# Performance work log

Measured on AMD Instinct MI355X. Metric: run time of the kernel, lower is better.

Reference implementation:

```python
import jax, jax.numpy as jnp
import numpy as np

N_NODES = 30000
N_EDGES = 480000
IN_FEAT = 256
OUT_FEAT = 256
N_RELS = 8
N_HEADS = 4
HEAD_DIM = OUT_FEAT // N_HEADS
LEAKY_SLOPE = 0.2


def setup_inputs() -> dict:
    key = jax.random.key(0)
    ks = jax.random.split(key, 8)
    inputs = jax.random.normal(ks[0], (N_NODES, IN_FEAT), dtype=jnp.float32)
    conv_weights = jax.random.normal(ks[1], (N_RELS, N_HEADS, IN_FEAT, HEAD_DIM), dtype=jnp.float32) * (1.0 / np.sqrt(IN_FEAT))
    attn_l = jax.random.normal(ks[2], (N_RELS, N_HEADS, HEAD_DIM), dtype=jnp.float32) * 0.1
    attn_r = jax.random.normal(ks[3], (N_RELS, N_HEADS, HEAD_DIM), dtype=jnp.float32) * 0.1
    h_bias = jax.random.normal(ks[4], (OUT_FEAT,), dtype=jnp.float32) * 0.02
    edge_src = jax.random.randint(ks[5], (N_EDGES,), 0, N_NODES, dtype=jnp.int32)
    edge_dst = jax.random.randint(ks[6], (N_EDGES,), 0, N_NODES, dtype=jnp.int32)
    edge_type = jax.random.randint(ks[7], (N_EDGES,), 0, N_RELS, dtype=jnp.int32)
    return {"inputs": inputs, "conv_weights": conv_weights, "attn_l": attn_l,
            "attn_r": attn_r, "h_bias": h_bias, "edge_src": edge_src,
            "edge_dst": edge_dst, "edge_type": edge_type}


def reference(inputs, conv_weights, attn_l, attn_r, h_bias, edge_src, edge_dst, edge_type):
    # Per-relation dense transform of all node features: [R, N, H, D]
    feat_all = jnp.einsum('ni,rhid->rnhd', inputs, conv_weights)
    # Gather transformed source/destination features per edge: [E, H, D]
    feat_src_e = feat_all[edge_type, edge_src]
    feat_dst_e = feat_all[edge_type, edge_dst]
    # Per-edge attention logits (relation-specific attn vectors): [E, H]
    el = jnp.sum(feat_src_e * attn_l[edge_type], axis=-1)
    er = jnp.sum(feat_dst_e * attn_r[edge_type], axis=-1)
    e = jax.nn.leaky_relu(el + er, negative_slope=LEAKY_SLOPE)
    # Segment softmax over incoming edges of each destination node
    m = jax.ops.segment_max(e, edge_dst, num_segments=N_NODES)  # [N, H]
    ex = jnp.exp(e - m[edge_dst])
    denom = jax.ops.segment_sum(ex, edge_dst, num_segments=N_NODES)  # [N, H]
    alpha = ex / denom[edge_dst]  # [E, H]
    # Attention-weighted aggregation of transformed source features
    h = jax.ops.segment_sum(alpha[..., None] * feat_src_e, edge_dst, num_segments=N_NODES)  # [N, H, D]
    h = h.reshape(N_NODES, OUT_FEAT) + h_bias
    # activation=None, self_loop=False, dropout=0.0 (eval) -> identity
    return h
```

## Files before the change

### kernel.cpp

```cpp
#include <hip/hip_runtime.h>

#define N_NODES 30000
#define NPAD    30080
#define N_EDGES 480000
#define N_RELS  8
#define NB_SCAN 118

typedef short bf16x8 __attribute__((ext_vector_type(8)));
typedef float f32x4  __attribute__((ext_vector_type(4)));

__device__ __forceinline__ unsigned short f2bf(float f) {
    unsigned u = __float_as_uint(f);
    u += 0x7fffu + ((u >> 16) & 1u);
    return (unsigned short)(u >> 16);
}
__device__ __forceinline__ float bf2f(unsigned short h) {
    return __uint_as_float(((unsigned)h) << 16);
}

__device__ __forceinline__ void load_lds16(const void* g, void* l) {
    __builtin_amdgcn_global_load_lds(
        (const __attribute__((address_space(1))) unsigned int*)g,
        (__attribute__((address_space(3))) unsigned int*)l,
        16, 0, 0);
}

__global__ void cast_x_kernel(const float* __restrict__ x, unsigned short* __restrict__ xbf) {
    int t = blockIdx.x * 256 + threadIdx.x;
    int base = t * 8;
    int n = base >> 8;
    unsigned short h[8];
    if (n < N_NODES) {
        float4 a = *(const float4*)(x + base);
        float4 b = *(const float4*)(x + base + 4);
        h[0]=f2bf(a.x); h[1]=f2bf(a.y); h[2]=f2bf(a.z); h[3]=f2bf(a.w);
        h[4]=f2bf(b.x); h[5]=f2bf(b.y); h[6]=f2bf(b.z); h[7]=f2bf(b.w);
    } else {
        #pragma unroll
        for (int i = 0; i < 8; ++i) h[i] = 0;
    }
    uint4 o;
    o.x = (unsigned)h[0] | ((unsigned)h[1] << 16);
    o.y = (unsigned)h[2] | ((unsigned)h[3] << 16);
    o.z = (unsigned)h[4] | ((unsigned)h[5] << 16);
    o.w = (unsigned)h[6] | ((unsigned)h[7] << 16);
    *(uint4*)(xbf + base) = o;
}

__global__ void wtrans_kernel(const float* __restrict__ cw, unsigned short* __restrict__ wt) {
    int o = blockIdx.x * 256 + threadIdx.x;
    if (o >= N_RELS * 256 * 256) return;
    int i = o & 255;
    int c = (o >> 8) & 255;
    int r = o >> 16;
    float v = cw[(((size_t)r * 4 + (c >> 6)) * 256 + i) * 64 + (c & 63)];
    wt[o] = f2bf(v);
}

__global__ void hist_kernel(const int* __restrict__ edst, int* __restrict__ counts) {
    int e = blockIdx.x * 256 + threadIdx.x;
    if (e < N_EDGES) atomicAdd(&counts[edst[e]], 1);
}

__global__ void scan1_kernel(const int* __restrict__ counts, int* __restrict__ locexcl,
                             int* __restrict__ bsum) {
    __shared__ int sm[256];
    int tid = threadIdx.x;
    int idx = blockIdx.x * 256 + tid;
    int v = (idx < N_NODES) ? counts[idx] : 0;
    sm[tid] = v;
    __syncthreads();
    for (int o = 1; o < 256; o <<= 1) {
        int t = (tid >= o) ? sm[tid - o] : 0;
        __syncthreads();
        sm[tid] += t;
        __syncthreads();
    }
    int incl = sm[tid];
    if (idx < N_NODES) locexcl[idx] = incl - v;
    if (tid == 255) bsum[blockIdx.x] = incl;
}

__global__ void scan2_kernel(const int* __restrict__ bsum, int* __restrict__ bpre) {
    __shared__ int sm[128];
    int tid = threadIdx.x;
    int v = (tid < NB_SCAN) ? bsum[tid] : 0;
    sm[tid] = v;
    __syncthreads();
    for (int o = 1; o < 128; o <<= 1) {
        int t = (tid >= o) ? sm[tid - o] : 0;
        __syncthreads();
        sm[tid] += t;
        __syncthreads();
    }
    if (tid < NB_SCAN) bpre[tid] = sm[tid] - v;
}

__global__ void scan3_kernel(const int* __restrict__ locexcl, const int* __restrict__ bpre,
                             int* __restrict__ offsets, int* __restrict__ cursor) {
    int idx = blockIdx.x * 256 + threadIdx.x;
    if (idx < N_NODES) {
        int o = bpre[blockIdx.x] + locexcl[idx];
        offsets[idx] = o;
        cursor[idx]  = o;
    }
    if (idx == 0) offsets[N_NODES] = N_EDGES;
}

__global__ __launch_bounds__(256) void gemm_kernel(
    const unsigned short* __restrict__ xbf,
    const unsigned short* __restrict__ wt,
    const float* __restrict__ attn_l,
    const float* __restrict__ attn_r,
    unsigned short* __restrict__ feat,
    float* __restrict__ projl,
    float* __restrict__ projr)
{
    __shared__ __align__(16) unsigned char smem[32768];

    const int tid  = threadIdx.x;
    const int lane = tid & 63;
    const int w    = tid >> 6;
    const int wm   = w >> 1;
    const int wn   = w & 1;
    const int quad = lane >> 4;
    const int l15  = lane & 15;

    const int bid = blockIdx.x;
    const int mt  = bid >> 4;
    const int r   = (bid >> 1) & 7;
    const int nt  = bid & 1;
    const int mbase = mt * 128;
    const int nbase = nt * 128;

    const unsigned short* Asrc = xbf + (size_t)mbase * 256;
    const unsigned short* Bsrc = wt + ((size_t)r * 256 + nbase) * 256;

    f32x4 acc[4][4] = {};

    const int srow = w * 16 + (lane >> 2);
    const int c0   = lane & 3;

    for (int k0 = 0; k0 < 256; k0 += 32) {
        #pragma unroll
        for (int n = 0; n < 2; ++n) {
            int row = n * 64 + srow;
            int c   = c0 ^ ((row >> 1) & 3);
            load_lds16(Asrc + (size_t)row * 256 + k0 + c * 8, smem + (n * 256 + w * 64) * 16);
        }
        #pragma unroll
        for (int n = 0; n < 2; ++n) {
            int row = n * 64 + srow;
            int c   = c0 ^ ((row >> 1) & 3);
            load_lds16(Bsrc + (size_t)row * 256 + k0 + c * 8, smem + 8192 + (n * 256 + w * 64) * 16);
        }
        __syncthreads();

        bf16x8 af[4], bfr[4];
        #pragma unroll
        for (int i = 0; i < 4; ++i) {
            int row = wm * 64 + i * 16 + l15;
            int cc  = quad ^ ((row >> 1) & 3);
            af[i] = *(const bf16x8*)(smem + row * 64 + cc * 16);
        }
        #pragma unroll
        for (int j = 0; j < 4; ++j) {
            int row = wn * 64 + j * 16 + l15;
            int cc  = quad ^ ((row >> 1) & 3);
            bfr[j] = *(const bf16x8*)(smem + 8192 + row * 64 + cc * 16);
        }

        #pragma unroll
        for (int i = 0; i < 4; ++i)
            #pragma unroll
            for (int j = 0; j < 4; ++j)
                acc[i][j] = __builtin_amdgcn_mfma_f32_16x16x32_bf16(af[i], bfr[j], acc[i][j], 0, 0, 0);
        __syncthreads();
    }

    size_t obase = ((size_t)r * NPAD + mbase + wm * 64) * 256 + nbase + wn * 64;
    #pragma unroll
    for (int i = 0; i < 4; ++i)
        #pragma unroll
        for (int j = 0; j < 4; ++j)
            #pragma unroll
            for (int e = 0; e < 4; ++e)
                feat[obase + (size_t)(i * 16 + quad * 4 + e) * 256 + j * 16 + l15] = f2bf(acc[i][j][e]);

    const int head = nt * 2 + wn;
    float al[4], ar[4];
    #pragma unroll
    for (int j = 0; j < 4; ++j) {
        al[j] = attn_l[((size_t)r * 4 + head) * 64 + j * 16 + l15];
        ar[j] = attn_r[((size_t)r * 4 + head) * 64 + j * 16 + l15];
    }
    float* bufL = (float*)smem + w * 1024;
    float* bufR = (float*)(smem + 16384) + w * 1024;
    #pragma unroll
    for (int i = 0; i < 4; ++i)
        #pragma unroll
        for (int e = 0; e < 4; ++e) {
            float s1 = 0.f, s2 = 0.f;
            #pragma unroll
            for (int j = 0; j < 4; ++j) {
                s1 += acc[i][j][e] * al[j];
                s2 += acc[i][j][e] * ar[j];
            }
            int row = i * 16 + quad * 4 + e;
            bufL[row * 16 + l15] = s1;
            bufR[row * 16 + l15] = s2;
        }
    float sL = 0.f, sR = 0.f;
    #pragma unroll
    for (int c = 0; c < 4; ++c) {
        float4 vl = *(const float4*)(bufL + lane * 16 + c * 4);
        float4 vr = *(const float4*)(bufR + lane * 16 + c * 4);
        sL += (vl.x + vl.y) + (vl.z + vl.w);
        sR += (vr.x + vr.y) + (vr.z + vr.w);
    }
    int g = mbase + wm * 64 + lane;
    projl[((size_t)r * NPAD + g) * 4 + head] = sL;
    projr[((size_t)r * NPAD + g) * 4 + head] = sR;
}

__global__ void logits_scatter_kernel(
    const int* __restrict__ esrc, const int* __restrict__ edst, const int* __restrict__ etyp,
    const float* __restrict__ projl, const float* __restrict__ projr,
    int* __restrict__ cursor, int* __restrict__ srcoff, float* __restrict__ exw)
{
    int e = blockIdx.x * 256 + threadIdx.x;
    if (e >= N_EDGES) return;
    int s = esrc[e], d = edst[e], t = etyp[e];
    float4 pl = ((const float4*)projl)[(size_t)t * NPAD + s];
    float4 pr = ((const float4*)projr)[(size_t)t * NPAD + d];
    float4 o;
    float v;
    v = pl.x + pr.x; v = v > 0.f ? v : 0.2f * v; o.x = __expf(v);
    v = pl.y + pr.y; v = v > 0.f ? v : 0.2f * v; o.y = __expf(v);
    v = pl.z + pr.z; v = v > 0.f ? v : 0.2f * v; o.z = __expf(v);
    v = pl.w + pr.w; v = v > 0.f ? v : 0.2f * v; o.w = __expf(v);
    int p = atomicAdd(&cursor[d], 1);
    srcoff[p] = t * NPAD + s;
    ((float4*)exw)[p] = o;
}

__global__ __launch_bounds__(256) void aggregate_kernel(
    const int* __restrict__ offsets, const int* __restrict__ srcoff,
    const float* __restrict__ exw, const unsigned short* __restrict__ feat,
    const float* __restrict__ bias, float* __restrict__ out)
{
    int v = blockIdx.x * 4 + (threadIdx.x >> 6);
    int lane = threadIdx.x & 63;
    int head = lane >> 4;
    int s0 = offsets[v], s1 = offsets[v + 1];
    float a0 = 0.f, a1 = 0.f, a2 = 0.f, a3 = 0.f, den = 0.f;
    int i = s0;
    for (; i + 4 <= s1; i += 4) {
        int o0 = srcoff[i], o1 = srcoff[i + 1], o2 = srcoff[i + 2], o3 = srcoff[i + 3];
        float e0 = exw[(size_t)i * 4 + head];
        float e1 = exw[(size_t)(i + 1) * 4 + head];
        float e2 = exw[(size_t)(i + 2) * 4 + head];
        float e3 = exw[(size_t)(i + 3) * 4 + head];
        ushort4 f0 = *(const ushort4*)(feat + (size_t)o0 * 256 + lane * 4);
        ushort4 f1 = *(const ushort4*)(feat + (size_t)o1 * 256 + lane * 4);
        ushort4 f2 = *(const ushort4*)(feat + (size_t)o2 * 256 + lane * 4);
        ushort4 f3 = *(const ushort4*)(feat + (size_t)o3 * 256 + lane * 4);
        den += (e0 + e1) + (e2 + e3);
        a0 += e0 * bf2f(f0.x) + e1 * bf2f(f1.x) + e2 * bf2f(f2.x) + e3 * bf2f(f3.x);
        a1 += e0 * bf2f(f0.y) + e1 * bf2f(f1.y) + e2 * bf2f(f2.y) + e3 * bf2f(f3.y);
        a2 += e0 * bf2f(f0.z) + e1 * bf2f(f1.z) + e2 * bf2f(f2.z) + e3 * bf2f(f3.z);
        a3 += e0 * bf2f(f0.w) + e1 * bf2f(f1.w) + e2 * bf2f(f2.w) + e3 * bf2f(f3.w);
    }
    for (; i < s1; ++i) {
        int o0 = srcoff[i];
        float e0 = exw[(size_t)i * 4 + head];
        ushort4 f0 = *(const ushort4*)(feat + (size_t)o0 * 256 + lane * 4);
        den += e0;
        a0 += e0 * bf2f(f0.x);
        a1 += e0 * bf2f(f0.y);
        a2 += e0 * bf2f(f0.z);
        a3 += e0 * bf2f(f0.w);
    }
    float inv = den > 0.f ? 1.f / den : 0.f;
    float4 o;
    o.x = a0 * inv + bias[lane * 4 + 0];
    o.y = a1 * inv + bias[lane * 4 + 1];
    o.z = a2 * inv + bias[lane * 4 + 2];
    o.w = a3 * inv + bias[lane * 4 + 3];
    ((float4*)out)[(size_t)v * 64 + lane] = o;
}

extern "C" void kernel_launch(void* const* d_in, const int* in_sizes, int n_in,
                              void* d_out, int out_size, void* d_ws, size_t ws_size,
                              hipStream_t stream) {
    const float* x    = (const float*)d_in[0];
    const float* cw   = (const float*)d_in[1];
    const float* al   = (const float*)d_in[2];
    const float* ar   = (const float*)d_in[3];
    const float* bias = (const float*)d_in[4];
    const int* esrc   = (const int*)d_in[5];
    const int* edst   = (const int*)d_in[6];
    const int* etyp   = (const int*)d_in[7];
    float* out        = (float*)d_out;

    char* ws = (char*)d_ws;
    size_t off = 0;
    auto alloc = [&](size_t bytes) { size_t o = off; off += (bytes + 255) & ~(size_t)255; return o; };

    unsigned short* xbf  = (unsigned short*)(ws + alloc((size_t)NPAD * 256 * 2));
    unsigned short* wt   = (unsigned short*)(ws + alloc((size_t)N_RELS * 256 * 256 * 2));
    unsigned short* feat = (unsigned short*)(ws + alloc((size_t)N_RELS * NPAD * 256 * 2));
    float* projl = (float*)(ws + alloc((size_t)N_RELS * NPAD * 4 * 4));
    float* projr = (float*)(ws + alloc((size_t)N_RELS * NPAD * 4 * 4));
    float* exw   = (float*)(ws + alloc((size_t)N_EDGES * 4 * 4));
    int* srcoff  = (int*)(ws + alloc((size_t)N_EDGES * 4));
    int* counts  = (int*)(ws + alloc((size_t)N_NODES * 4));
    int* offsets = (int*)(ws + alloc((size_t)(N_NODES + 1) * 4));
    int* cursor  = (int*)(ws + alloc((size_t)N_NODES * 4));
    int* locexcl = (int*)(ws + alloc((size_t)N_NODES * 4));
    int* bsum    = (int*)(ws + alloc((size_t)NB_SCAN * 4));
    int* bpre    = (int*)(ws + alloc((size_t)NB_SCAN * 4));

    hipMemsetAsync(counts, 0, (size_t)N_NODES * 4, stream);

    cast_x_kernel<<<3760, 256, 0, stream>>>(x, xbf);
    wtrans_kernel<<<2048, 256, 0, stream>>>(cw, wt);
    hist_kernel<<<1875, 256, 0, stream>>>(edst, counts);
    scan1_kernel<<<NB_SCAN, 256, 0, stream>>>(counts, locexcl, bsum);
    scan2_kernel<<<1, 128, 0, stream>>>(bsum, bpre);
    scan3_kernel<<<NB_SCAN, 256, 0, stream>>>(locexcl, bpre, offsets, cursor);
    gemm_kernel<<<3760, 256, 0, stream>>>(xbf, wt, al, ar, feat, projl, projr);
    logits_scatter_kernel<<<1875, 256, 0, stream>>>(esrc, edst, etyp, projl, projr,
                                                    cursor, srcoff, exw);
    aggregate_kernel<<<7500, 256, 0, stream>>>(offsets, srcoff, exw, feat, bias, out);
}
```

Before: 258.7 us.

## Merge prep kernels, transpose GEMM MFMA for vector stores, deepen aggregate unroll

Merges the three preprocessing kernels (x cast, weight transpose, degree histogram) into a single launch split by block index, cutting launch overhead. Swaps the MFMA operand order in the GEMM so each lane holds four consecutive output features and can write them as ushort4 vectors instead of scalar bf16 stores. The attention projection reduction is reworked to match, using a padded stride-5 LDS buffer. The aggregate gather loop is unrolled to 8 edges, with 4 and 2 edge tails, so more loads are in flight, at the cost of more registers.

```diff
diff --git a/kernel.cpp b/kernel.cpp
--- a/kernel.cpp
+++ b/kernel.cpp
@@ -25,41 +25,41 @@
         16, 0, 0);
 }
 
-__global__ void cast_x_kernel(const float* __restrict__ x, unsigned short* __restrict__ xbf) {
-    int t = blockIdx.x * 256 + threadIdx.x;
-    int base = t * 8;
-    int n = base >> 8;
-    unsigned short h[8];
-    if (n < N_NODES) {
-        float4 a = *(const float4*)(x + base);
-        float4 b = *(const float4*)(x + base + 4);
-        h[0]=f2bf(a.x); h[1]=f2bf(a.y); h[2]=f2bf(a.z); h[3]=f2bf(a.w);
-        h[4]=f2bf(b.x); h[5]=f2bf(b.y); h[6]=f2bf(b.z); h[7]=f2bf(b.w);
+__global__ void prep_kernel(const float* __restrict__ x, unsigned short* __restrict__ xbf,
+                            const float* __restrict__ cw, unsigned short* __restrict__ wt,
+                            const int* __restrict__ edst, int* __restrict__ counts) {
+    int b = blockIdx.x;
+    if (b < 3760) {
+        int t = b * 256 + threadIdx.x;
+        int base = t * 8;
+        int n = base >> 8;
+        unsigned short h[8];
+        if (n < N_NODES) {
+            float4 a = *(const float4*)(x + base);
+            float4 c = *(const float4*)(x + base + 4);
+            h[0]=f2bf(a.x); h[1]=f2bf(a.y); h[2]=f2bf(a.z); h[3]=f2bf(a.w);
+            h[4]=f2bf(c.x); h[5]=f2bf(c.y); h[6]=f2bf(c.z); h[7]=f2bf(c.w);
+        } else {
+            #pragma unroll
+            for (int i = 0; i < 8; ++i) h[i] = 0;
+        }
+        uint4 o;
+        o.x = (unsigned)h[0] | ((unsigned)h[1] << 16);
+        o.y = (unsigned)h[2] | ((unsigned)h[3] << 16);
+        o.z = (unsigned)h[4] | ((unsigned)h[5] << 16);
+        o.w = (unsigned)h[6] | ((unsigned)h[7] << 16);
+        *(uint4*)(xbf + base) = o;
+    } else if (b < 5808) {
+        int o = (b - 3760) * 256 + threadIdx.x;
+        int i = o & 255;
+        int c = (o >> 8) & 255;
+        int r = o >> 16;
+        float v = cw[(((size_t)r * 4 + (c >> 6)) * 256 + i) * 64 + (c & 63)];
+        wt[o] = f2bf(v);
     } else {
-        #pragma unroll
-        for (int i = 0; i < 8; ++i) h[i] = 0;
-    }
-    uint4 o;
-    o.x = (unsigned)h[0] | ((unsigned)h[1] << 16);
-    o.y = (unsigned)h[2] | ((unsigned)h[3] << 16);
-    o.z = (unsigned)h[4] | ((unsigned)h[5] << 16);
-    o.w = (unsigned)h[6] | ((unsigned)h[7] << 16);
-    *(uint4*)(xbf + base) = o;
-}
-
-__global__ void wtrans_kernel(const float* __restrict__ cw, unsigned short* __restrict__ wt) {
-    int o = blockIdx.x * 256 + threadIdx.x;
-    if (o >= N_RELS * 256 * 256) return;
-    int i = o & 255;
-    int c = (o >> 8) & 255;
-    int r = o >> 16;
-    float v = cw[(((size_t)r * 4 + (c >> 6)) * 256 + i) * 64 + (c & 63)];
-    wt[o] = f2bf(v);
-}
-
-__global__ void hist_kernel(const int* __restrict__ edst, int* __restrict__ counts) {
-    int e = blockIdx.x * 256 + threadIdx.x;
-    if (e < N_EDGES) atomicAdd(&counts[edst[e]], 1);
+        int e = (b - 5808) * 256 + threadIdx.x;
+        if (e < N_EDGES) atomicAdd(&counts[edst[e]], 1);
+    }
 }
 
 __global__ void scan1_kernel(const int* __restrict__ counts, int* __restrict__ locexcl,
@@ -156,67 +156,74 @@
         }
         __syncthreads();
 
-        bf16x8 af[4], bfr[4];
+        bf16x8 xf[4], wf[4];
+        #pragma unroll
+        for (int j = 0; j < 4; ++j) {
+            int row = wm * 64 + j * 16 + l15;
+            int cc  = quad ^ ((row >> 1) & 3);
+            xf[j] = *(const bf16x8*)(smem + row * 64 + cc * 16);
+        }
         #pragma unroll
         for (int i = 0; i < 4; ++i) {
-            int row = wm * 64 + i * 16 + l15;
+            int row = wn * 64 + i * 16 + l15;
             int cc  = quad ^ ((row >> 1) & 3);
-            af[i] = *(const bf16x8*)(smem + row * 64 + cc * 16);
-        }
-        #pragma unroll
-        for (int j = 0; j < 4; ++j) {
-            int row = wn * 64 + j * 16 + l15;
-            int cc  = quad ^ ((row >> 1) & 3);
-            bfr[j] = *(const bf16x8*)(smem + 8192 + row * 64 + cc * 16);
+            wf[i] = *(const bf16x8*)(smem + 8192 + row * 64 + cc * 16);
         }
 
         #pragma unroll
         for (int i = 0; i < 4; ++i)
             #pragma unroll
             for (int j = 0; j < 4; ++j)
-                acc[i][j] = __builtin_amdgcn_mfma_f32_16x16x32_bf16(af[i], bfr[j], acc[i][j], 0, 0, 0);
-        __syncthreads();
-    }
-
-    size_t obase = ((size_t)r * NPAD + mbase + wm * 64) * 256 + nbase + wn * 64;
+                acc[i][j] = __builtin_amdgcn_mfma_f32_16x16x32_bf16(wf[i], xf[j], acc[i][j], 0, 0, 0);
+        __syncthreads();
+    }
+
+    #pragma unroll
+    for (int j = 0; j < 4; ++j) {
+        int node = mbase + wm * 64 + j * 16 + l15;
+        size_t rowb = ((size_t)r * NPAD + node) * 256 + nbase + wn * 64;
+        #pragma unroll
+        for (int i = 0; i < 4; ++i) {
+            ushort4 v;
+            v.x = f2bf(acc[i][j][0]);
+            v.y = f2bf(acc[i][j][1]);
+            v.z = f2bf(acc[i][j][2]);
+            v.w = f2bf(acc[i][j][3]);
+            *(ushort4*)(feat + rowb + i * 16 + quad * 4) = v;
+        }
+    }
+
+    const int head = nt * 2 + wn;
+    float alv[4][4], arv[4][4];
     #pragma unroll
     for (int i = 0; i < 4; ++i)
         #pragma unroll
-        for (int j = 0; j < 4; ++j)
-            #pragma unroll
-            for (int e = 0; e < 4; ++e)
-                feat[obase + (size_t)(i * 16 + quad * 4 + e) * 256 + j * 16 + l15] = f2bf(acc[i][j][e]);
-
-    const int head = nt * 2 + wn;
-    float al[4], ar[4];
-    #pragma unroll
-    for (int j = 0; j < 4; ++j) {
-        al[j] = attn_l[((size_t)r * 4 + head) * 64 + j * 16 + l15];
-        ar[j] = attn_r[((size_t)r * 4 + head) * 64 + j * 16 + l15];
-    }
+        for (int e = 0; e < 4; ++e) {
+            int c = i * 16 + quad * 4 + e;
+            alv[i][e] = attn_l[((size_t)r * 4 + head) * 64 + c];
+            arv[i][e] = attn_r[((size_t)r * 4 + head) * 64 + c];
+        }
     float* bufL = (float*)smem + w * 1024;
     float* bufR = (float*)(smem + 16384) + w * 1024;
     #pragma unroll
-    for (int i = 0; i < 4; ++i)
-        #pragma unroll
-        for (int e = 0; e < 4; ++e) {
-            float s1 = 0.f, s2 = 0.f;
+    for (int j = 0; j < 4; ++j) {
+        float s1 = 0.f, s2 = 0.f;
+        #pragma unroll
+        for (int i = 0; i < 4; ++i)
             #pragma unroll
-            for (int j = 0; j < 4; ++j) {
-                s1 += acc[i][j][e] * al[j];
-                s2 += acc[i][j][e] * ar[j];
+            for (int e = 0; e < 4; ++e) {
+                s1 += acc[i][j][e] * alv[i][e];
+                s2 += acc[i][j][e] * arv[i][e];
             }
-            int row = i * 16 + quad * 4 + e;
-            bufL[row * 16 + l15] = s1;
-            bufR[row * 16 + l15] = s2;
-        }
+        int node = j * 16 + l15;
+        bufL[node * 5 + quad] = s1;
+        bufR[node * 5 + quad] = s2;
+    }
     float sL = 0.f, sR = 0.f;
     #pragma unroll
-    for (int c = 0; c < 4; ++c) {
-        float4 vl = *(const float4*)(bufL + lane * 16 + c * 4);
-        float4 vr = *(const float4*)(bufR + lane * 16 + c * 4);
-        sL += (vl.x + vl.y) + (vl.z + vl.w);
-        sR += (vr.x + vr.y) + (vr.z + vr.w);
+    for (int q = 0; q < 4; ++q) {
+        sL += bufL[lane * 5 + q];
+        sR += bufR[lane * 5 + q];
     }
     int g = mbase + wm * 64 + lane;
     projl[((size_t)r * NPAD + g) * 4 + head] = sL;
@@ -255,23 +262,52 @@
     int s0 = offsets[v], s1 = offsets[v + 1];
     float a0 = 0.f, a1 = 0.f, a2 = 0.f, a3 = 0.f, den = 0.f;
     int i = s0;
+    for (; i + 8 <= s1; i += 8) {
+        int o[8]; float ee[8]; ushort4 ff[8];
+        #pragma unroll
+        for (int u = 0; u < 8; ++u) { o[u] = srcoff[i + u]; ee[u] = exw[(size_t)(i + u) * 4 + head]; }
+        #pragma unroll
+        for (int u = 0; u < 8; ++u) ff[u] = *(const ushort4*)(feat + (size_t)o[u] * 256 + lane * 4);
+        #pragma unroll
+        for (int u = 0; u < 8; ++u) {
+            den += ee[u];
+            a0 += ee[u] * bf2f(ff[u].x);
+            a1 += ee[u] * bf2f(ff[u].y);
+            a2 += ee[u] * bf2f(ff[u].z);
+            a3 += ee[u] * bf2f(ff[u].w);
+        }
+    }
     for (; i + 4 <= s1; i += 4) {
-        int o0 = srcoff[i], o1 = srcoff[i + 1], o2 = srcoff[i + 2], o3 = srcoff[i + 3];
-        float e0 = exw[(size_t)i * 4 + head];
-        float e1 = exw[(size_t)(i + 1) * 4 + head];
-        float e2 = exw[(size_t)(i + 2) * 4 + head];
-        float e3 = exw[(size_t)(i + 3) * 4 + head];
-        ushort4 f0 = *(const ushort4*)(feat + (size_t)o0 * 256 + lane * 4);
-        ushort4 f1 = *(const ushort4*)(feat + (size_t)o1 * 256 + lane * 4);
-        ushort4 f2 = *(const ushort4*)(feat + (size_t)o2 * 256 + lane * 4);
-        ushort4 f3 = *(const ushort4*)(feat + (size_t)o3 * 256 + lane * 4);
-        den += (e0 + e1) + (e2 + e3);
-        a0 += e0 * bf2f(f0.x) + e1 * bf2f(f1.x) + e2 * bf2f(f2.x) + e3 * bf2f(f3.x);
-        a1 += e0 * bf2f(f0.y) + e1 * bf2f(f1.y) + e2 * bf2f(f2.y) + e3 * bf2f(f3.y);
-        a2 += e0 * bf2f(f0.z) + e1 * bf2f(f1.z) + e2 * bf2f(f2.z) + e3 * bf2f(f3.z);
-        a3 += e0 * bf2f(f0.w) + e1 * bf2f(f1.w) + e2 * bf2f(f2.w) + e3 * bf2f(f3.w);
-    }
-    for (; i < s1; ++i) {
+        int o[4]; float ee[4]; ushort4 ff[4];
+        #pragma unroll
+        for (int u = 0; u < 4; ++u) { o[u] = srcoff[i + u]; ee[u] = exw[(size_t)(i + u) * 4 + head]; }
+        #pragma unroll
+        for (int u = 0; u < 4; ++u) ff[u] = *(const ushort4*)(feat + (size_t)o[u] * 256 + lane * 4);
+        #pragma unroll
+        for (int u = 0; u < 4; ++u) {
+            den += ee[u];
+            a0 += ee[u] * bf2f(ff[u].x);
+            a1 += ee[u] * bf2f(ff[u].y);
+            a2 += ee[u] * bf2f(ff[u].z);
+            a3 += ee[u] * bf2f(ff[u].w);
+        }
+    }
+    for (; i + 2 <= s1; i += 2) {
+        int o[2]; float ee[2]; ushort4 ff[2];
+        #pragma unroll
+        for (int u = 0; u < 2; ++u) { o[u] = srcoff[i + u]; ee[u] = exw[(size_t)(i + u) * 4 + head]; }
+        #pragma unroll
+        for (int u = 0; u < 2; ++u) ff[u] = *(const ushort4*)(feat + (size_t)o[u] * 256 + lane * 4);
+        #pragma unroll
+        for (int u = 0; u < 2; ++u) {
+            den += ee[u];
+            a0 += ee[u] * bf2f(ff[u].x);
+            a1 += ee[u] * bf2f(ff[u].y);
+            a2 += ee[u] * bf2f(ff[u].z);
+            a3 += ee[u] * bf2f(ff[u].w);
+        }
+    }
+    if (i < s1) {
         int o0 = srcoff[i];
         float e0 = exw[(size_t)i * 4 + head];
         ushort4 f0 = *(const ushort4*)(feat + (size_t)o0 * 256 + lane * 4);
@@ -323,9 +359,7 @@
 
     hipMemsetAsync(counts, 0, (size_t)N_NODES * 4, stream);
 
-    cast_x_kernel<<<3760, 256, 0, stream>>>(x, xbf);
-    wtrans_kernel<<<2048, 256, 0, stream>>>(cw, wt);
-    hist_kernel<<<1875, 256, 0, stream>>>(edst, counts);
+    prep_kernel<<<7683, 256, 0, stream>>>(x, xbf, cw, wt, edst, counts);
     scan1_kernel<<<NB_SCAN, 256, 0, stream>>>(counts, locexcl, bsum);
     scan2_kernel<<<1, 128, 0, stream>>>(bsum, bpre);
     scan3_kernel<<<NB_SCAN, 256, 0, stream>>>(locexcl, bpre, offsets, cursor);
```

Result: no change. 260.8 us (+0.8%).
